# Kernel optimization log

Hardware: AMD Instinct MI355X
Metric: run time of the kernel (lower is better)

The kernel has to match this reference:

```python
import jax, jax.numpy as jnp
import numpy as np

H = 1024  # hidden_size
IN = 1024  # input_size
EPS = 1e-05


def _ln(v):
    # LayerNorm over last dim, no affine (gamma/beta applied by caller)
    c = v - v.mean(-1, keepdims=True)
    return c * jax.lax.rsqrt((c * c).mean(-1, keepdims=True) + EPS)


def setup_inputs() -> dict:
    key = jax.random.key(0)
    ks = jax.random.split(key, 12)
    stdv = 1.0 / np.sqrt(IN + 2 * H)
    u = lambda k, shape, s=stdv: jax.random.uniform(k, shape, jnp.float32, -s, s)
    bias = jnp.zeros((4 * H,), jnp.float32).at[:H].set(1.0)
    return {
        "input": jax.random.normal(ks[0], (512, 64, IN), jnp.float32),
        "hidden": jax.random.normal(ks[1], (64, H), jnp.float32),
        "cell": jax.random.normal(ks[2], (64, H), jnp.float32),
        "weight_ih": u(ks[3], (4 * H, IN)),
        "weight_hh": u(ks[4], (4 * H, H)),
        "weight_ch": u(ks[5], (3 * H,)),
        "bias": bias,
        "gamma_f": jax.random.uniform(ks[6], (H,), jnp.float32),
        "gamma_i": jax.random.uniform(ks[7], (H,), jnp.float32),
        "gamma_g": jax.random.uniform(ks[8], (H,), jnp.float32),
        "gamma_o": jax.random.uniform(ks[9], (H,), jnp.float32),
        "gamma_cell": jax.random.uniform(ks[10], (H,), jnp.float32),
        "beta_cell": jnp.zeros((H,), jnp.float32),
    }


def reference(input, hidden, cell, weight_ih, weight_hh, weight_ch, bias,
              gamma_f, gamma_i, gamma_g, gamma_o, gamma_cell, beta_cell):
    # input: [T, B, IN]; hidden/cell: [B, H]. Eval mode (dropout inactive).
    w_cf, w_ci, w_co = weight_ch[:H], weight_ch[H:2 * H], weight_ch[2 * H:]
    b_f, b_i, b_g, b_o = jnp.split(bias, 4)
    # Precompute input projections for all timesteps: [T, B, 4H]
    x_proj = jnp.einsum('tbi,gi->tbg', input, weight_ih)

    def step(carry, xp):
        h, c = carry
        gates = xp + h @ weight_hh.T  # [B, 4H]
        f_hat, i_hat, g_hat, o_hat = jnp.split(gates, 4, axis=-1)
        f = jax.nn.sigmoid(_ln(f_hat + w_cf * c) * gamma_f + b_f)
        i = jax.nn.sigmoid(_ln(i_hat + w_ci * c) * gamma_i + b_i)
        g = jnp.tanh(_ln(g_hat) * gamma_g + b_g)
        c_new = f * c + i * g
        c_ln = _ln(c_new) * gamma_cell + beta_cell
        o = jax.nn.sigmoid(_ln(o_hat + w_co * c_new) * gamma_o + b_o)
        h_new = o * jnp.tanh(c_ln)
        return (h_new, c_new), h_new

    (h_f, c_f), out = jax.lax.scan(step, (hidden, cell), x_proj)
    return out, h_f, c_f
```

## Files before the change

kernel.cpp:

```cpp
#include <hip/hip_runtime.h>

#define T_STEPS 512
#define BATCH   64
#define HID     1024
#define GDIM    4096
#define KDIM    2048
#define NGW     128
#define NSW     64
#define CWG     32
#define BHID    (BATCH * HID)

using short8  = __attribute__((ext_vector_type(8))) short;
using floatx4 = __attribute__((ext_vector_type(4))) float;
typedef unsigned long long u64;

__device__ inline unsigned short bf16_rne(float f) {
  union { float f; unsigned u; } x; x.f = f;
  unsigned r = x.u + 0x7FFFu + ((x.u >> 16) & 1u);
  return (unsigned short)(r >> 16);
}

__device__ inline float sigmoid_(float x) { return 1.0f / (1.0f + __expf(-x)); }
__device__ inline float tanh_(float x) {
  float e = __expf(-2.0f * fabsf(x));
  float r = (1.0f - e) / (1.0f + e);
  return copysignf(r, x);
}

#define LOAD4(dst, ptr) { float4 _t4 = *(const float4*)(ptr); \
  dst[0]=_t4.x; dst[1]=_t4.y; dst[2]=_t4.z; dst[3]=_t4.w; }

__device__ inline u64 ld_u64_mall(const void* p) {
  return __hip_atomic_load((const u64*)p, __ATOMIC_RELAXED, __HIP_MEMORY_SCOPE_AGENT);
}
__device__ inline void st_u64_mall(void* p, u64 v) {
  __hip_atomic_store((u64*)p, v, __ATOMIC_RELAXED, __HIP_MEMORY_SCOPE_AGENT);
}
__device__ inline void st_u32_mall(void* p, unsigned v) {
  __hip_atomic_store((unsigned*)p, v, __ATOMIC_RELAXED, __HIP_MEMORY_SCOPE_AGENT);
}
__device__ inline unsigned ld_u32_mall(const void* p) {
  return __hip_atomic_load((const unsigned*)p, __ATOMIC_RELAXED, __HIP_MEMORY_SCOPE_AGENT);
}
__device__ inline short8 ld_a16_mall(const unsigned short* p) {
  union { u64 q[2]; short8 v; } u;
  u.q[0] = ld_u64_mall(p);
  u.q[1] = ld_u64_mall(p + 4);
  return u.v;
}
__device__ inline void ld4f_mall(float* d, const float* p) {
  union { u64 q; float f[2]; } a, b;
  a.q = ld_u64_mall(p);
  b.q = ld_u64_mall(p + 2);
  d[0] = a.f[0]; d[1] = a.f[1]; d[2] = b.f[0]; d[3] = b.f[1];
}
__device__ inline void st4h_mall(unsigned short* p, float a, float b, float c, float d) {
  union { u64 q; unsigned short s[4]; } u;
  u.s[0] = bf16_rne(a); u.s[1] = bf16_rne(b); u.s[2] = bf16_rne(c); u.s[3] = bf16_rne(d);
  st_u64_mall(p, u.q);
}

__global__ __launch_bounds__(256) void cvt_w_kernel(
    const float* __restrict__ w_hh, const float* __restrict__ w_ih,
    unsigned short* __restrict__ wcat)
{
  int idx  = blockIdx.x * 256 + threadIdx.x;
  int base = idx * 4;
  int g = base >> 11;
  int k = base & 2047;
  const float* src = (k < 1024) ? (w_hh + (size_t)g * 1024 + k)
                                : (w_ih + (size_t)g * 1024 + (k - 1024));
  float a = src[0], b = src[1], c = src[2], d = src[3];
  uint2 v;
  v.x = (unsigned)bf16_rne(a) | ((unsigned)bf16_rne(b) << 16);
  v.y = (unsigned)bf16_rne(c) | ((unsigned)bf16_rne(d) << 16);
  *(uint2*)(wcat + base) = v;
}

__global__ __launch_bounds__(256) void cvt_x_kernel(
    const float* __restrict__ x, unsigned short* __restrict__ xall)
{
  size_t i = ((size_t)blockIdx.x * 256 + threadIdx.x) * 8;
  float4 a = *(const float4*)(x + i);
  float4 b = *(const float4*)(x + i + 4);
  union { unsigned short s[8]; uint4 v; } u;
  u.s[0] = bf16_rne(a.x); u.s[1] = bf16_rne(a.y); u.s[2] = bf16_rne(a.z); u.s[3] = bf16_rne(a.w);
  u.s[4] = bf16_rne(b.x); u.s[5] = bf16_rne(b.y); u.s[6] = bf16_rne(b.z); u.s[7] = bf16_rne(b.w);
  *(uint4*)(xall + i) = u.v;
}

__global__ __launch_bounds__(256) void init_kernel(
    const float* __restrict__ hidden, const float* __restrict__ x0,
    const float* __restrict__ cell,
    unsigned short* __restrict__ hdst, unsigned short* __restrict__ xdst,
    float* __restrict__ c_ws)
{
  const int b = blockIdx.x;
  const int j = threadIdx.x * 4;
  const size_t off = (size_t)b * HID + j;
  float4 h = *(const float4*)(hidden + off);
  float4 x = *(const float4*)(x0 + off);
  float4 c = *(const float4*)(cell + off);
  ushort4 hv, xv;
  hv.x = bf16_rne(h.x); hv.y = bf16_rne(h.y); hv.z = bf16_rne(h.z); hv.w = bf16_rne(h.w);
  xv.x = bf16_rne(x.x); xv.y = bf16_rne(x.y); xv.z = bf16_rne(x.z); xv.w = bf16_rne(x.w);
  *(ushort4*)(hdst + off) = hv;
  *(ushort4*)(xdst + off) = xv;
  *(float4*)(c_ws + off) = c;
}

template<int N>
__device__ inline void block_reduce(float* v, float* red, int tid) {
#pragma unroll
  for (int i = 0; i < N; ++i) {
    float x = v[i];
#pragma unroll
    for (int off = 32; off > 0; off >>= 1)
      x += __shfl_xor(x, off, 64);
    v[i] = x;
  }
  const int wave = tid >> 6;
  if ((tid & 63) == 0) {
#pragma unroll
    for (int i = 0; i < N; ++i) red[wave * N + i] = v[i];
  }
  __syncthreads();
#pragma unroll
  for (int i = 0; i < N; ++i)
    v[i] = red[i] + red[N + i] + red[2 * N + i] + red[3 * N + i];
}

#define MFMA16(a, b, c) __builtin_amdgcn_mfma_f32_16x16x32_bf16(a, b, c, 0, 0, 0)

template<int MODE>
__global__ __launch_bounds__(256, 1) void lstm_persist(
    const unsigned short* __restrict__ wcat,
    const float* __restrict__ input,
    const unsigned short* __restrict__ xA,
    unsigned short* __restrict__ xbuf,
    float* __restrict__ gates, float* __restrict__ c_ws,
    const float* __restrict__ w_ch, const float* __restrict__ bias,
    const float* __restrict__ gamma_f, const float* __restrict__ gamma_i,
    const float* __restrict__ gamma_g, const float* __restrict__ gamma_o,
    const float* __restrict__ gamma_c, const float* __restrict__ beta_c,
    float* __restrict__ out,
    unsigned short* __restrict__ hA,
    unsigned* __restrict__ syncp)
{
  __shared__ __align__(16) unsigned short smB[CWG * KDIM];
  __shared__ float sm[40];

  const int wg   = blockIdx.x;
  const int tid  = threadIdx.x;
  const int wave = tid >> 6;
  const int lane = tid & 63;
  const int quad = lane >> 4;
  const int l16  = lane & 15;

  unsigned* gflags = syncp;
  unsigned* hflags = syncp + 512;

  const floatx4 z = {0.f, 0.f, 0.f, 0.f};

  if (wg < NGW) {
    const int n0 = wg * CWG;
    for (int i = 0; i < 32; ++i) {
      int idx = wave * 32 + i;
      int t2 = idx >> 6, kc = idx & 63;
      short8 v = *(const short8*)(wcat + (size_t)(n0 + t2 * 16 + l16) * KDIM
                                  + kc * 32 + quad * 8);
      *(short8*)(smB + (size_t)idx * 512 + lane * 8) = v;
    }
    __syncthreads();

    const size_t rowoff = (size_t)(wave * 16 + l16) * HID + quad * 8;

    for (int t = 0; t < T_STEPS; ++t) {
      floatx4 x0e = z, x1e = z, x0o = z, x1o = z;
      if (MODE >= 1) {
        const unsigned short* ax = xA + (size_t)t * BHID + rowoff;
#pragma unroll
        for (int kc = 0; kc < 32; kc += 2) {
          short8 ae  = *(const short8*)(ax + kc * 32);
          short8 ao  = *(const short8*)(ax + (kc + 1) * 32);
          short8 b0e = *(const short8*)(smB + (size_t)(32 + kc) * 512 + lane * 8);
          short8 b1e = *(const short8*)(smB + (size_t)(96 + kc) * 512 + lane * 8);
          short8 b0o = *(const short8*)(smB + (size_t)(33 + kc) * 512 + lane * 8);
          short8 b1o = *(const short8*)(smB + (size_t)(97 + kc) * 512 + lane * 8);
          x0e = MFMA16(ae, b0e, x0e); x1e = MFMA16(ae, b1e, x1e);
          x0o = MFMA16(ao, b0o, x0o); x1o = MFMA16(ao, b1o, x1o);
        }
      }

      if (tid < NSW) {
        const unsigned* fp = hflags + tid;
        while (ld_u32_mall(fp) < (unsigned)t) { }
      }
      __syncthreads();

      if (MODE == 0) {
#pragma unroll
        for (int kc = 0; kc < 32; kc += 2) {
          short8 ae  = ld_a16_mall(xA + rowoff + kc * 32);
          short8 ao  = ld_a16_mall(xA + rowoff + (kc + 1) * 32);
          short8 b0e = *(const short8*)(smB + (size_t)(32 + kc) * 512 + lane * 8);
          short8 b1e = *(const short8*)(smB + (size_t)(96 + kc) * 512 + lane * 8);
          short8 b0o = *(const short8*)(smB + (size_t)(33 + kc) * 512 + lane * 8);
          short8 b1o = *(const short8*)(smB + (size_t)(97 + kc) * 512 + lane * 8);
          x0e = MFMA16(ae, b0e, x0e); x1e = MFMA16(ae, b1e, x1e);
          x0o = MFMA16(ao, b0o, x0o); x1o = MFMA16(ao, b1o, x1o);
        }
      }

      short8 aH[32];
      if (MODE == 2) {
        const unsigned short* ah = hA + (size_t)t * BHID + rowoff;
#pragma unroll
        for (int kc = 0; kc < 32; ++kc)
          aH[kc] = *(const short8*)(ah + kc * 32);
      } else {
#pragma unroll
        for (int kc = 0; kc < 32; ++kc)
          aH[kc] = ld_a16_mall(hA + rowoff + kc * 32);
      }

      floatx4 h0e = z, h1e = z, h0o = z, h1o = z;
#pragma unroll
      for (int kc = 0; kc < 32; kc += 2) {
        short8 b0e = *(const short8*)(smB + (size_t)kc * 512 + lane * 8);
        short8 b1e = *(const short8*)(smB + (size_t)(64 + kc) * 512 + lane * 8);
        short8 b0o = *(const short8*)(smB + (size_t)(kc + 1) * 512 + lane * 8);
        short8 b1o = *(const short8*)(smB + (size_t)(65 + kc) * 512 + lane * 8);
        h0e = MFMA16(aH[kc],     b0e, h0e); h1e = MFMA16(aH[kc],     b1e, h1e);
        h0o = MFMA16(aH[kc + 1], b0o, h0o); h1o = MFMA16(aH[kc + 1], b1o, h1o);
      }

#pragma unroll
      for (int r = 0; r < 4; ++r) {
        int m = wave * 16 + quad * 4 + r;
        float* gm = gates + (size_t)m * GDIM + n0 + l16;
        st_u32_mall(gm,      __float_as_uint((h0e[r] + h0o[r]) + (x0e[r] + x0o[r])));
        st_u32_mall(gm + 16, __float_as_uint((h1e[r] + h1o[r]) + (x1e[r] + x1o[r])));
      }
      asm volatile("s_waitcnt vmcnt(0)" ::: "memory");
      __syncthreads();
      if (tid == 0)
        st_u32_mall(gflags + wg, (unsigned)(t + 1));
    }
  } else {
    const int b = wg - NGW;
    const int j = tid * 4;

    float cc[4], wcf[4], wci[4], wco[4];
    float gf4[4], gi4[4], gg4[4], go4[4], gc4[4], bc4[4];
    float bf4[4], bi4[4], bg4[4], bo4[4];
    LOAD4(cc,  c_ws + (size_t)b * HID + j);
    LOAD4(wcf, w_ch + j);
    LOAD4(wci, w_ch + HID + j);
    LOAD4(wco, w_ch + 2 * HID + j);
    LOAD4(gf4, gamma_f + j); LOAD4(gi4, gamma_i + j);
    LOAD4(gg4, gamma_g + j); LOAD4(go4, gamma_o + j);
    LOAD4(gc4, gamma_c + j); LOAD4(bc4, beta_c + j);
    LOAD4(bf4, bias + j);           LOAD4(bi4, bias + HID + j);
    LOAD4(bg4, bias + 2 * HID + j); LOAD4(bo4, bias + 3 * HID + j);
    const float invH = 1.0f / (float)HID;

    for (int t = 0; t < T_STEPS; ++t) {
      const int has_next = (t + 1 < T_STEPS);
      float4 xv;
      if (MODE == 0 && has_next)
        xv = *(const float4*)(input + (size_t)(t + 1) * BHID + (size_t)b * HID + j);

      if (tid < NGW) {
        const unsigned* fp = gflags + tid;
        while (ld_u32_mall(fp) < (unsigned)(t + 1)) { }
      }
      __syncthreads();

      float fh[4], ih[4], gh[4], oh[4];
      const float* grow = gates + (size_t)b * GDIM;
      ld4f_mall(fh, grow + j);
      ld4f_mall(ih, grow + HID + j);
      ld4f_mall(gh, grow + 2 * HID + j);
      ld4f_mall(oh, grow + 3 * HID + j);

      if (MODE == 0 && has_next)
        st4h_mall(xbuf + (size_t)b * HID + j, xv.x, xv.y, xv.z, xv.w);

      float af[4], ai[4], ag[4];
      float s[6] = {0, 0, 0, 0, 0, 0};
#pragma unroll
      for (int r = 0; r < 4; ++r) {
        af[r] = fh[r] + wcf[r] * cc[r];
        ai[r] = ih[r] + wci[r] * cc[r];
        ag[r] = gh[r];
        s[0] += af[r]; s[1] += af[r] * af[r];
        s[2] += ai[r]; s[3] += ai[r] * ai[r];
        s[4] += ag[r]; s[5] += ag[r] * ag[r];
      }
      block_reduce<6>(s, sm, tid);
      float mu_f = s[0] * invH, is_f = rsqrtf(s[1] * invH - mu_f * mu_f + 1e-5f);
      float mu_i = s[2] * invH, is_i = rsqrtf(s[3] * invH - mu_i * mu_i + 1e-5f);
      float mu_g = s[4] * invH, is_g = rsqrtf(s[5] * invH - mu_g * mu_g + 1e-5f);

      float cn[4], ao[4];
      float s2[4] = {0, 0, 0, 0};
#pragma unroll
      for (int r = 0; r < 4; ++r) {
        float f = sigmoid_((af[r] - mu_f) * is_f * gf4[r] + bf4[r]);
        float i = sigmoid_((ai[r] - mu_i) * is_i * gi4[r] + bi4[r]);
        float g = tanh_((ag[r] - mu_g) * is_g * gg4[r] + bg4[r]);
        cn[r] = f * cc[r] + i * g;
        ao[r] = oh[r] + wco[r] * cn[r];
        s2[0] += cn[r]; s2[1] += cn[r] * cn[r];
        s2[2] += ao[r]; s2[3] += ao[r] * ao[r];
      }
#pragma unroll
      for (int r = 0; r < 4; ++r) cc[r] = cn[r];

      block_reduce<4>(s2, sm + 24, tid);
      float mu_c = s2[0] * invH, is_c = rsqrtf(s2[1] * invH - mu_c * mu_c + 1e-5f);
      float mu_o = s2[2] * invH, is_o = rsqrtf(s2[3] * invH - mu_o * mu_o + 1e-5f);

      float h4[4];
#pragma unroll
      for (int r = 0; r < 4; ++r) {
        float cl = (cn[r] - mu_c) * is_c * gc4[r] + bc4[r];
        float o  = sigmoid_((ao[r] - mu_o) * is_o * go4[r] + bo4[r]);
        h4[r] = o * tanh_(cl);
      }
      { float4 tt; tt.x = h4[0]; tt.y = h4[1]; tt.z = h4[2]; tt.w = h4[3];
        *(float4*)(out + (size_t)t * BHID + (size_t)b * HID + j) = tt; }
      if (has_next) {
        unsigned short* hd = (MODE == 2)
            ? hA + (size_t)(t + 1) * BHID + (size_t)b * HID + j
            : hA + (size_t)b * HID + j;
        st4h_mall(hd, h4[0], h4[1], h4[2], h4[3]);
      }

      asm volatile("s_waitcnt vmcnt(0)" ::: "memory");
      __syncthreads();
      if (tid == 0)
        st_u32_mall(hflags + b, (unsigned)(t + 1));
    }

    { float4 tt; tt.x = cc[0]; tt.y = cc[1]; tt.z = cc[2]; tt.w = cc[3];
      *(float4*)(c_ws + (size_t)b * HID + j) = tt; }
  }
}

extern "C" void kernel_launch(void* const* d_in, const int* in_sizes, int n_in,
                              void* d_out, int out_size, void* d_ws, size_t ws_size,
                              hipStream_t stream) {
  (void)in_sizes; (void)n_in; (void)out_size;
  const float* input   = (const float*)d_in[0];
  const float* hidden  = (const float*)d_in[1];
  const float* cell    = (const float*)d_in[2];
  const float* w_ih    = (const float*)d_in[3];
  const float* w_hh    = (const float*)d_in[4];
  const float* w_ch    = (const float*)d_in[5];
  const float* bias    = (const float*)d_in[6];
  const float* gamma_f = (const float*)d_in[7];
  const float* gamma_i = (const float*)d_in[8];
  const float* gamma_g = (const float*)d_in[9];
  const float* gamma_o = (const float*)d_in[10];
  const float* gamma_c = (const float*)d_in[11];
  const float* beta_c  = (const float*)d_in[12];
  float* out = (float*)d_out;

  const size_t SZ_WCAT = (size_t)GDIM * KDIM * sizeof(unsigned short);
  const size_t SZ_XALL = (size_t)T_STEPS * BHID * sizeof(unsigned short);
  const size_t SZ_HPOOL= (size_t)T_STEPS * BHID * sizeof(unsigned short);
  const size_t SZ_BUF  = (size_t)BHID * sizeof(unsigned short);
  const size_t SZ_GATE = (size_t)BATCH * GDIM * sizeof(float);
  const size_t SZ_VEC  = (size_t)BHID * sizeof(float);
  const size_t SZ_FLAG = 16384;
  const size_t TAIL = SZ_GATE + SZ_VEC + SZ_FLAG;
  const size_t NEED2 = SZ_WCAT + SZ_XALL + SZ_HPOOL + TAIL;
  const size_t NEED1 = SZ_WCAT + SZ_XALL + SZ_BUF + TAIL;

  char* p = (char*)d_ws;
  unsigned short* wcat = (unsigned short*)p;  p += SZ_WCAT;
  int mode = (ws_size >= NEED2) ? 2 : (ws_size >= NEED1) ? 1 : 0;

  unsigned short *xA, *xbuf, *hA;
  if (mode >= 1) {
    xA = (unsigned short*)p; p += SZ_XALL; xbuf = xA;
    hA = (unsigned short*)p; p += (mode == 2) ? SZ_HPOOL : SZ_BUF;
  } else {
    xA = (unsigned short*)p; p += SZ_BUF;  xbuf = xA;
    hA = (unsigned short*)p; p += SZ_BUF;
  }
  float* gates = (float*)p;  p += SZ_GATE;
  float* c_ws  = (float*)p;  p += SZ_VEC;
  unsigned* syncp = (unsigned*)p;

  cvt_w_kernel<<<(GDIM * KDIM / 4) / 256, 256, 0, stream>>>(w_hh, w_ih, wcat);
  if (mode >= 1)
    cvt_x_kernel<<<((size_t)T_STEPS * BHID / 8) / 256, 256, 0, stream>>>(input, xA);
  init_kernel<<<BATCH, 256, 0, stream>>>(hidden, input, cell, hA, xA, c_ws);
  hipMemsetAsync(syncp, 0, SZ_FLAG, stream);

  if (mode == 2)
    lstm_persist<2><<<NGW + NSW, 256, 0, stream>>>(
        wcat, input, xA, xbuf, gates, c_ws, w_ch, bias, gamma_f, gamma_i,
        gamma_g, gamma_o, gamma_c, beta_c, out, hA, syncp);
  else if (mode == 1)
    lstm_persist<1><<<NGW + NSW, 256, 0, stream>>>(
        wcat, input, xA, xbuf, gates, c_ws, w_ch, bias, gamma_f, gamma_i,
        gamma_g, gamma_o, gamma_c, beta_c, out, hA, syncp);
  else
    lstm_persist<0><<<NGW + NSW, 256, 0, stream>>>(
        wcat, input, xA, xbuf, gates, c_ws, w_ch, bias, gamma_f, gamma_i,
        gamma_g, gamma_o, gamma_c, beta_c, out, hA, syncp);

  const size_t OUT0 = (size_t)T_STEPS * BHID;
  hipMemcpyAsync(out + OUT0, out + (OUT0 - BHID),
                 (size_t)BHID * sizeof(float), hipMemcpyDeviceToDevice, stream);
  hipMemcpyAsync(out + OUT0 + BHID, c_ws,
                 (size_t)BHID * sizeof(float), hipMemcpyDeviceToDevice, stream);
}
```

Before: 7.010 ms.

## Replace block-level flag barriers with per-wave flags in persistent LSTM kernel

Cross-workgroup signalling moves from one flag per workgroup, which needed __syncthreads before publishing, to one flag per wave. Each wave now waits only on the specific producer waves whose data it reads. The output store and the xbuf store are reordered so the h flag is published before the big fp32 output write. The intent is to cut barrier latency on the serial recurrence critical path, at the cost of more flags to poll and a more delicate correctness argument about which waves depend on which.

```diff
diff --git a/kernel.cpp b/kernel.cpp
--- a/kernel.cpp
+++ b/kernel.cpp
@@ -157,8 +157,8 @@
   const int quad = lane >> 4;
   const int l16  = lane & 15;
 
-  unsigned* gflags = syncp;
-  unsigned* hflags = syncp + 512;
+  unsigned* gwflags = syncp;
+  unsigned* hwflags = syncp + 512;
 
   const floatx4 z = {0.f, 0.f, 0.f, 0.f};
 
@@ -174,6 +174,7 @@
     __syncthreads();
 
     const size_t rowoff = (size_t)(wave * 16 + l16) * HID + quad * 8;
+    const unsigned* hfp = hwflags + 64 * wave + lane;
 
     for (int t = 0; t < T_STEPS; ++t) {
       floatx4 x0e = z, x1e = z, x0o = z, x1o = z;
@@ -192,11 +193,9 @@
         }
       }
 
-      if (tid < NSW) {
-        const unsigned* fp = hflags + tid;
-        while (ld_u32_mall(fp) < (unsigned)t) { }
-      }
-      __syncthreads();
+      if (t > 0) {
+        while (ld_u32_mall(hfp) < (unsigned)t) { }
+      }
 
       if (MODE == 0) {
 #pragma unroll
@@ -243,13 +242,15 @@
         st_u32_mall(gm + 16, __float_as_uint((h1e[r] + h1o[r]) + (x1e[r] + x1o[r])));
       }
       asm volatile("s_waitcnt vmcnt(0)" ::: "memory");
-      __syncthreads();
-      if (tid == 0)
-        st_u32_mall(gflags + wg, (unsigned)(t + 1));
+      if (lane == 0)
+        st_u32_mall(gwflags + wave * 128 + wg, (unsigned)(t + 1));
     }
   } else {
     const int b = wg - NGW;
     const int j = tid * 4;
+
+    const unsigned* gfp = gwflags + (b >> 4) * 128
+                        + ((lane >> 3) * 32 + wave * 8 + (lane & 7));
 
     float cc[4], wcf[4], wci[4], wco[4];
     float gf4[4], gi4[4], gg4[4], go4[4], gc4[4], bc4[4];
@@ -271,11 +272,9 @@
       if (MODE == 0 && has_next)
         xv = *(const float4*)(input + (size_t)(t + 1) * BHID + (size_t)b * HID + j);
 
-      if (tid < NGW) {
-        const unsigned* fp = gflags + tid;
-        while (ld_u32_mall(fp) < (unsigned)(t + 1)) { }
-      }
-      __syncthreads();
+      if (lane < 32) {
+        while (ld_u32_mall(gfp) < (unsigned)(t + 1)) { }
+      }
 
       float fh[4], ih[4], gh[4], oh[4];
       const float* grow = gates + (size_t)b * GDIM;
@@ -283,9 +282,6 @@
       ld4f_mall(ih, grow + HID + j);
       ld4f_mall(gh, grow + 2 * HID + j);
       ld4f_mall(oh, grow + 3 * HID + j);
-
-      if (MODE == 0 && has_next)
-        st4h_mall(xbuf + (size_t)b * HID + j, xv.x, xv.y, xv.z, xv.w);
 
       float af[4], ai[4], ag[4];
       float s[6] = {0, 0, 0, 0, 0, 0};
@@ -329,19 +325,20 @@
         float o  = sigmoid_((ao[r] - mu_o) * is_o * go4[r] + bo4[r]);
         h4[r] = o * tanh_(cl);
       }
-      { float4 tt; tt.x = h4[0]; tt.y = h4[1]; tt.z = h4[2]; tt.w = h4[3];
-        *(float4*)(out + (size_t)t * BHID + (size_t)b * HID + j) = tt; }
+
       if (has_next) {
         unsigned short* hd = (MODE == 2)
             ? hA + (size_t)(t + 1) * BHID + (size_t)b * HID + j
             : hA + (size_t)b * HID + j;
         st4h_mall(hd, h4[0], h4[1], h4[2], h4[3]);
-      }
-
-      asm volatile("s_waitcnt vmcnt(0)" ::: "memory");
-      __syncthreads();
-      if (tid == 0)
-        st_u32_mall(hflags + b, (unsigned)(t + 1));
+        if (MODE == 0)
+          st4h_mall(xbuf + (size_t)b * HID + j, xv.x, xv.y, xv.z, xv.w);
+        asm volatile("s_waitcnt vmcnt(0)" ::: "memory");
+        if (lane == 0)
+          st_u32_mall(hwflags + b * 4 + wave, (unsigned)(t + 1));
+      }
+      { float4 tt; tt.x = h4[0]; tt.y = h4[1]; tt.z = h4[2]; tt.w = h4[3];
+        *(float4*)(out + (size_t)t * BHID + (size_t)b * HID + j) = tt; }
     }
 
     { float4 tt; tt.x = cc[0]; tt.y = cc[1]; tt.z = cc[2]; tt.w = cc[3];
```

Result: slower. 7.854 ms (+12.0%).
